# Optimization experiments

Measured on AMD Instinct MI355X. Metric: run time of the kernel, lower is better.

The kernel has to match this reference:

```python
import jax, jax.numpy as jnp
import numpy as np

COST_MASK = 5.0
COST_DICE = 5.0
COST_BOX = 5.0
COST_GIOU = 2.0


def point_sample(masks, pts):
    # masks: [N, H, W]; pts: [P, 2] with (x, y) in [0, 1].
    # Matches F.grid_sample(bilinear, align_corners=False, padding_mode='zeros')
    N, H, W = masks.shape
    x = pts[:, 0] * W - 0.5
    y = pts[:, 1] * H - 0.5
    x0 = jnp.floor(x)
    y0 = jnp.floor(y)
    wx = x - x0
    wy = y - y0
    x0i = x0.astype(jnp.int32)
    y0i = y0.astype(jnp.int32)

    def gather(yi, xi):
        valid = ((xi >= 0) & (xi < W) & (yi >= 0) & (yi < H)).astype(masks.dtype)
        v = masks[:, jnp.clip(yi, 0, H - 1), jnp.clip(xi, 0, W - 1)]  # [N, P]
        return v * valid

    v00 = gather(y0i, x0i)
    v01 = gather(y0i, x0i + 1)
    v10 = gather(y0i + 1, x0i)
    v11 = gather(y0i + 1, x0i + 1)
    return (v00 * (1 - wy) * (1 - wx) + v01 * (1 - wy) * wx
            + v10 * wy * (1 - wx) + v11 * wy * wx)  # [N, P]


def box_cxcywh_to_xyxy(b):
    cx, cy, w, h = b[..., 0], b[..., 1], b[..., 2], b[..., 3]
    return jnp.stack([cx - 0.5 * w, cy - 0.5 * h, cx + 0.5 * w, cy + 0.5 * h], axis=-1)


def generalized_box_iou(a, b):
    # a: [Q, 4], b: [T, 4] in xyxy
    area_a = (a[:, 2] - a[:, 0]) * (a[:, 3] - a[:, 1])
    area_b = (b[:, 2] - b[:, 0]) * (b[:, 3] - b[:, 1])
    lt = jnp.maximum(a[:, None, :2], b[None, :, :2])
    rb = jnp.minimum(a[:, None, 2:], b[None, :, 2:])
    wh = jnp.clip(rb - lt, 0.0)
    inter = wh[..., 0] * wh[..., 1]
    union = area_a[:, None] + area_b[None, :] - inter
    iou = inter / union
    lt_e = jnp.minimum(a[:, None, :2], b[None, :, :2])
    rb_e = jnp.maximum(a[:, None, 2:], b[None, :, 2:])
    wh_e = jnp.clip(rb_e - lt_e, 0.0)
    area_e = wh_e[..., 0] * wh_e[..., 1]
    return iou - (area_e - union) / area_e


def _cost_one(out_mask, tgt_mask, out_box, tgt_box, pts):
    om = point_sample(out_mask, pts)  # [Q, P] logits
    tm = point_sample(tgt_mask, pts)  # [T, P] binary targets
    P = om.shape[1]
    # batch_sigmoid_ce_loss: BCE(x,1)=softplus(-x), BCE(x,0)=softplus(x)
    pos = jax.nn.softplus(-om)
    neg = jax.nn.softplus(om)
    cost_mask = (jnp.einsum('qp,tp->qt', pos, tm)
                 + jnp.einsum('qp,tp->qt', neg, 1.0 - tm)) / P
    # batch_dice_loss
    s = jax.nn.sigmoid(om)
    numerator = 2.0 * jnp.einsum('qp,tp->qt', s, tm)
    denominator = s.sum(-1)[:, None] + tm.sum(-1)[None, :]
    cost_dice = 1.0 - (numerator + 1.0) / (denominator + 1.0)
    # box costs
    cost_bbox = jnp.abs(out_box[:, None, :] - tgt_box[None, :, :]).sum(-1)
    cost_giou = -generalized_box_iou(box_cxcywh_to_xyxy(out_box),
                                     box_cxcywh_to_xyxy(tgt_box))
    return (COST_MASK * cost_mask + COST_DICE * cost_dice
            + COST_BOX * cost_bbox + COST_GIOU * cost_giou)


def setup_inputs() -> dict:
    key = jax.random.key(0)
    k1, k2, k3, k4, k5 = jax.random.split(key, 5)
    B, Q, T, H, W, P = 2, 300, 300, 256, 256, 12544
    pred_masks = jax.random.normal(k1, (B, Q, H, W), dtype=jnp.float32)
    tgt_masks = (jax.random.uniform(k2, (B, T, H, W)) > 0.5).astype(jnp.float32)
    u = jax.random.uniform(k3, (B, Q, 4), dtype=jnp.float32)
    pred_boxes = jnp.concatenate([0.2 + 0.6 * u[..., :2], 0.05 + 0.25 * u[..., 2:]], axis=-1)
    v = jax.random.uniform(k4, (B, T, 4), dtype=jnp.float32)
    tgt_boxes = jnp.concatenate([0.2 + 0.6 * v[..., :2], 0.05 + 0.25 * v[..., 2:]], axis=-1)
    point_coords = jax.random.uniform(k5, (B, P, 2), dtype=jnp.float32)
    return {"pred_masks": pred_masks, "tgt_masks": tgt_masks,
            "pred_boxes": pred_boxes, "tgt_boxes": tgt_boxes,
            "point_coords": point_coords}


def reference(pred_masks, tgt_masks, pred_boxes, tgt_boxes, point_coords):
    # Batched cost matrix C: [B, Q, T]
    return jax.vmap(_cost_one)(pred_masks, tgt_masks, pred_boxes, tgt_boxes, point_coords)
```

## Files before the change

### kernel.cpp

```cpp
#include <hip/hip_runtime.h>
#include <hip/hip_bf16.h>
#include <math.h>

#define BB 2
#define QQ 300
#define TT 300
#define HH 256
#define WW 256
#define PP 12544
#define NCHUNK 16
#define PBLK (PP / 256)
#define NSPLIT 14

typedef __bf16 bf16_t;
typedef bf16_t bf16x8 __attribute__((ext_vector_type(8)));
typedef float floatx4 __attribute__((ext_vector_type(4)));

__device__ inline void gl_lds16(const void* g, void* l) {
    __builtin_amdgcn_global_load_lds(
        (const __attribute__((address_space(1))) unsigned int*)g,
        (__attribute__((address_space(3))) unsigned int*)l, 16, 0, 0);
}

#define LG_BAR() do {                                      \
    __builtin_amdgcn_sched_barrier(0);                     \
    asm volatile("s_waitcnt lgkmcnt(0)" ::: "memory");     \
    __builtin_amdgcn_s_barrier();                          \
    __builtin_amdgcn_sched_barrier(0);                     \
} while (0)

#define VM_BAR(N) do {                                     \
    __builtin_amdgcn_sched_barrier(0);                     \
    asm volatile("s_waitcnt vmcnt(" #N ")" ::: "memory");  \
    __builtin_amdgcn_s_barrier();                          \
    __builtin_amdgcn_sched_barrier(0);                     \
} while (0)

__global__ __launch_bounds__(256) void prep_kernel(const float* __restrict__ pts,
                                                   int4* __restrict__ off,
                                                   float4* __restrict__ wgt,
                                                   int* __restrict__ bkt,
                                                   int* __restrict__ hist) {
    __shared__ int lh[NCHUNK];
    int tid = threadIdx.x;
    if (tid < NCHUNK) lh[tid] = 0;
    __syncthreads();
    int idx = blockIdx.x * 256 + tid;
    int b = blockIdx.x / PBLK;
    float px = pts[idx * 2 + 0];
    float py = pts[idx * 2 + 1];
    float x = px * WW - 0.5f;
    float y = py * HH - 0.5f;
    float x0f = floorf(x), y0f = floorf(y);
    float wx = x - x0f, wy = y - y0f;
    int x0 = (int)x0f, y0 = (int)y0f;
    int x1 = x0 + 1, y1 = y0 + 1;
    float vx0 = (x0 >= 0 && x0 < WW) ? 1.f : 0.f;
    float vx1 = (x1 >= 0 && x1 < WW) ? 1.f : 0.f;
    float vy0 = (y0 >= 0 && y0 < HH) ? 1.f : 0.f;
    float vy1 = (y1 >= 0 && y1 < HH) ? 1.f : 0.f;
    int cx0 = min(max(x0, 0), WW - 1), cx1 = min(max(x1, 0), WW - 1);
    int cy0 = min(max(y0, 0), HH - 1), cy1 = min(max(y1, 0), HH - 1);
    off[idx] = make_int4(cy0 * WW + cx0, cy0 * WW + cx1, cy1 * WW + cx0, cy1 * WW + cx1);
    wgt[idx] = make_float4((1.f - wy) * (1.f - wx) * vy0 * vx0,
                           (1.f - wy) * wx        * vy0 * vx1,
                           wy        * (1.f - wx) * vy1 * vx0,
                           wy        * wx         * vy1 * vx1);
    int k = min(max(y0, 0), HH - 2) >> 4;
    bkt[idx] = k;
    atomicAdd(&lh[k], 1);
    __syncthreads();
    if (tid < NCHUNK && lh[tid] > 0) atomicAdd(&hist[b * NCHUNK + tid], lh[tid]);
}

__global__ void scan_kernel(const int* __restrict__ hist, int* __restrict__ cs,
                            int* __restrict__ ctr) {
    int b = threadIdx.x;
    if (b < BB) {
        int run = 0;
        for (int k = 0; k < NCHUNK; ++k) {
            cs[b * (NCHUNK + 1) + k] = run;
            ctr[b * NCHUNK + k] = run;
            run += hist[b * NCHUNK + k];
        }
        cs[b * (NCHUNK + 1) + NCHUNK] = run;
    }
}

__global__ __launch_bounds__(256) void scatter_kernel(const int4* __restrict__ off,
                                                      const float4* __restrict__ wgt,
                                                      const int* __restrict__ bkt,
                                                      int* __restrict__ ctr,
                                                      int4* __restrict__ off_s,
                                                      float4* __restrict__ wgt_s) {
    __shared__ int lh[NCHUNK];
    __shared__ int lbase[NCHUNK];
    int tid = threadIdx.x;
    if (tid < NCHUNK) lh[tid] = 0;
    __syncthreads();
    int idx = blockIdx.x * 256 + tid;
    int b = blockIdx.x / PBLK;
    int k = bkt[idx];
    int rank = atomicAdd(&lh[k], 1);
    __syncthreads();
    if (tid < NCHUNK) lbase[tid] = (lh[tid] > 0) ? atomicAdd(&ctr[b * NCHUNK + tid], lh[tid]) : 0;
    __syncthreads();
    int pos = lbase[k] + rank;
    off_s[b * PP + pos] = off[idx];
    wgt_s[b * PP + pos] = wgt[idx];
}

__global__ __launch_bounds__(256) void sample_kernel(
    const float* __restrict__ pred_masks, const float* __restrict__ tgt_masks,
    const int4* __restrict__ off_s, const float4* __restrict__ wgt_s,
    const int* __restrict__ cs_g,
    bf16_t* __restrict__ OM, bf16_t* __restrict__ TM,
    float* __restrict__ RS_SP, float* __restrict__ RS_S, float* __restrict__ RS_T) {
    int b = blockIdx.z;
    int m = blockIdx.x;
    int c = blockIdx.y;
    int tid = threadIdx.x;
    int wave = tid >> 6, lane = tid & 63;
    __shared__ __align__(16) float rows[17 * WW];
    __shared__ float ra_[4], rb_[4];

    bool is_pred = (m < QQ);
    const float* img;
    bf16_t* row0;
    if (is_pred) {
        img  = pred_masks + (size_t)(b * QQ + m) * (HH * WW);
        row0 = OM + (size_t)(b * QQ + m) * PP;
    } else {
        int t = m - QQ;
        img  = tgt_masks + (size_t)(b * TT + t) * (HH * WW);
        row0 = TM + (size_t)(b * TT + t) * PP;
    }

    int base = c * 16;
    const float4* gsrc = (const float4*)(img + base * WW);
    float4 p0 = gsrc[(wave + 0) * 64 + lane];
    float4 p1 = gsrc[(wave + 4) * 64 + lane];
    float4 p2 = gsrc[(wave + 8) * 64 + lane];
    float4 p3 = gsrc[(wave + 12) * 64 + lane];
    float4 p4;
    bool has17 = (c < NCHUNK - 1);
    if (has17 && wave == 0) p4 = gsrc[16 * 64 + lane];

    const int4*   offb = off_s + b * PP;
    const float4* wb   = wgt_s + b * PP;
    const int*    cs   = cs_g + b * (NCHUNK + 1);
    int j1 = cs[c + 1];
    int j = cs[c] + tid;
    int4 o; float4 w;
    if (j < j1) { o = offb[j]; w = wb[j]; }

    float4* d = (float4*)rows;
    d[(wave + 0) * 64 + lane] = p0;
    d[(wave + 4) * 64 + lane] = p1;
    d[(wave + 8) * 64 + lane] = p2;
    d[(wave + 12) * 64 + lane] = p3;
    if (has17 && wave == 0) d[16 * 64 + lane] = p4;
    __syncthreads();

    int boff = base * WW;
    float s0 = 0.f, s1 = 0.f;
    while (j < j1) {
        int jn = j + 256;
        int4 on; float4 wn;
        if (jn < j1) { on = offb[jn]; wn = wb[jn]; }
        float v = w.x * rows[o.x - boff] + w.y * rows[o.y - boff] +
                  w.z * rows[o.z - boff] + w.w * rows[o.w - boff];
        row0[j] = (bf16_t)v;
        if (is_pred) {
            float e = __expf(-fabsf(v));
            float r = 1.f / (1.f + e);
            float sg = (v >= 0.f) ? r : e * r;
            s0 += fmaxf(v, 0.f) + __logf(1.f + e);
            s1 += sg;
        } else {
            s0 += v;
        }
        o = on; w = wn; j = jn;
    }

    for (int sh = 32; sh > 0; sh >>= 1) {
        s0 += __shfl_down(s0, sh, 64);
        s1 += __shfl_down(s1, sh, 64);
    }
    if (lane == 0) { ra_[wave] = s0; rb_[wave] = s1; }
    __syncthreads();
    if (tid == 0) {
        float t0 = ra_[0] + ra_[1] + ra_[2] + ra_[3];
        float t1 = rb_[0] + rb_[1] + rb_[2] + rb_[3];
        if (is_pred) {
            atomicAdd(&RS_SP[b * QQ + m], t0);
            atomicAdd(&RS_S[b * QQ + m], t1);
        } else {
            atomicAdd(&RS_T[b * TT + (m - QQ)], t0);
        }
    }
}

__device__ inline bf16x8 sigmoid8(bf16x8 a) {
    bf16x8 r;
#pragma unroll
    for (int i = 0; i < 8; ++i) {
        float x = (float)a[i];
        float e = __expf(-fabsf(x));
        float q = 1.f / (1.f + e);
        r[i] = (bf16_t)((x >= 0.f) ? q : e * q);
    }
    return r;
}

template<int NS>
__global__ __launch_bounds__(512) void matmul_kernel(
    const bf16_t* __restrict__ OM, const bf16_t* __restrict__ TM,
    float* __restrict__ A1P, float* __restrict__ A2P) {
    constexpr int KSP = PP / NS;
    constexpr int KST = KSP / 64;
    static_assert(KSP % 64 == 0, "K split must be a multiple of 64");
    int b = blockIdx.z / NS;
    int split = blockIdx.z % NS;
    int m0 = blockIdx.x * 128;
    int n0 = blockIdx.y * 128;
    int tid = threadIdx.x;
    int wave = tid >> 6, lane = tid & 63;
    int lrow = lane & 15, quad = lane >> 4;
    int wm = wave & 3;
    int wn = wave >> 2;

    __shared__ __align__(16) bf16_t lds[2][2 * 128 * 64];

    int k0 = split * KSP;
    int lr8 = lane >> 3;
    int clog = (lane & 7) ^ lr8;

    const char* gp[4];
    unsigned lofs[4];
#pragma unroll
    for (int jj = 0; jj < 4; ++jj) {
        int L = wave + jj * 8;
        int mat = L >> 4, i = L & 15;
        int rb_ = mat ? n0 : m0;
        int row = min(rb_ + i * 8 + lr8, mat ? (TT - 1) : (QQ - 1));
        const bf16_t* g = mat ? TM + (size_t)b * TT * PP : OM + (size_t)b * QQ * PP;
        gp[jj] = (const char*)(g + (size_t)row * PP + k0) + clog * 16;
        lofs[jj] = mat * 8192 + i * 512;
    }

    floatx4 acc1[2][4], acc2[2][4];
#pragma unroll
    for (int r = 0; r < 2; ++r)
#pragma unroll
        for (int j = 0; j < 4; ++j) {
            acc1[r][j] = (floatx4){0.f, 0.f, 0.f, 0.f};
            acc2[r][j] = (floatx4){0.f, 0.f, 0.f, 0.f};
        }

#pragma unroll
    for (int jj = 0; jj < 4; ++jj) { gl_lds16(gp[jj], lds[0] + lofs[jj]); gp[jj] += 128; }

    int ar0 = wm * 32 + lrow;
    int ar1 = ar0 + 16;
    int ax0 = ar0 & 7, ax1 = ar1 & 7;
    for (int s = 0; s < KST; ++s) {
        if (s + 1 < KST) {
#pragma unroll
            for (int jj = 0; jj < 4; ++jj) { gl_lds16(gp[jj], lds[(s + 1) & 1] + lofs[jj]); gp[jj] += 128; }
            VM_BAR(4);
        } else {
            VM_BAR(0);
        }
        const bf16_t* Lp = lds[s & 1];
#pragma unroll
        for (int kk8 = 0; kk8 <= 4; kk8 += 4) {
            bf16x8 a1_0 = *(const bf16x8*)(Lp + ar0 * 64 + (((quad + kk8) ^ ax0) << 3));
            bf16x8 a1_1 = *(const bf16x8*)(Lp + ar1 * 64 + (((quad + kk8) ^ ax1) << 3));
            bf16x8 a2_0 = sigmoid8(a1_0);
            bf16x8 a2_1 = sigmoid8(a1_1);
#pragma unroll
            for (int j = 0; j < 4; ++j) {
                int br = wn * 64 + j * 16 + lrow;
                bf16x8 vb = *(const bf16x8*)(Lp + 8192 + br * 64 + (((quad + kk8) ^ (br & 7)) << 3));
                acc1[0][j] = __builtin_amdgcn_mfma_f32_16x16x32_bf16(a1_0, vb, acc1[0][j], 0, 0, 0);
                acc1[1][j] = __builtin_amdgcn_mfma_f32_16x16x32_bf16(a1_1, vb, acc1[1][j], 0, 0, 0);
                acc2[0][j] = __builtin_amdgcn_mfma_f32_16x16x32_bf16(a2_0, vb, acc2[0][j], 0, 0, 0);
                acc2[1][j] = __builtin_amdgcn_mfma_f32_16x16x32_bf16(a2_1, vb, acc2[1][j], 0, 0, 0);
            }
        }
        LG_BAR();
    }

    float* o1 = A1P + (size_t)(b * NS + split) * (QQ * TT);
    float* o2 = A2P + (size_t)(b * NS + split) * (QQ * TT);
#pragma unroll
    for (int r16 = 0; r16 < 2; ++r16) {
        int mrow = m0 + wm * 32 + r16 * 16 + quad * 4;
#pragma unroll
        for (int j = 0; j < 4; ++j) {
            int n = n0 + wn * 64 + j * 16 + lrow;
            if (n < TT) {
#pragma unroll
                for (int r = 0; r < 4; ++r) {
                    int mm = mrow + r;
                    if (mm < QQ) {
                        o1[mm * TT + n] = acc1[r16][j][r];
                        o2[mm * TT + n] = acc2[r16][j][r];
                    }
                }
            }
        }
    }
}

template<int NS>
__global__ __launch_bounds__(256) void combine_kernel(
    const float* __restrict__ A1P, const float* __restrict__ A2P,
    const float* __restrict__ RS_SP, const float* __restrict__ RS_S, const float* __restrict__ RS_T,
    const float* __restrict__ pred_boxes, const float* __restrict__ tgt_boxes,
    float* __restrict__ out) {
    int idx = blockIdx.x * 256 + threadIdx.x;
    if (idx >= BB * QQ * TT) return;
    int b = idx / (QQ * TT);
    int r = idx - b * (QQ * TT);
    int q = r / TT;
    int t = r - q * TT;

    float a1 = 0.f, a2 = 0.f;
    for (int s = 0; s < NS; ++s) {
        a1 += A1P[(size_t)(b * NS + s) * (QQ * TT) + r];
        a2 += A2P[(size_t)(b * NS + s) * (QQ * TT) + r];
    }
    float cm = (RS_SP[b * QQ + q] - a1) * (1.0f / (float)PP);
    float cd = 1.f - (2.f * a2 + 1.f) / (RS_S[b * QQ + q] + RS_T[b * TT + t] + 1.f);

    const float* pb = pred_boxes + (size_t)(b * QQ + q) * 4;
    const float* tb = tgt_boxes + (size_t)(b * TT + t) * 4;
    float cb = fabsf(pb[0] - tb[0]) + fabsf(pb[1] - tb[1]) +
               fabsf(pb[2] - tb[2]) + fabsf(pb[3] - tb[3]);

    float ax0 = pb[0] - 0.5f * pb[2], ay0 = pb[1] - 0.5f * pb[3];
    float ax1 = pb[0] + 0.5f * pb[2], ay1 = pb[1] + 0.5f * pb[3];
    float bx0 = tb[0] - 0.5f * tb[2], by0 = tb[1] - 0.5f * tb[3];
    float bx1 = tb[0] + 0.5f * tb[2], by1 = tb[1] + 0.5f * tb[3];
    float area_a = (ax1 - ax0) * (ay1 - ay0);
    float area_b = (bx1 - bx0) * (by1 - by0);
    float iw = fmaxf(fminf(ax1, bx1) - fmaxf(ax0, bx0), 0.f);
    float ih = fmaxf(fminf(ay1, by1) - fmaxf(ay0, by0), 0.f);
    float inter = iw * ih;
    float uni = area_a + area_b - inter;
    float iou = inter / uni;
    float ew = fmaxf(ax1, bx1) - fminf(ax0, bx0);
    float eh = fmaxf(ay1, by1) - fminf(ay0, by0);
    float area_e = ew * eh;
    float giou = iou - (area_e - uni) / area_e;

    out[idx] = 5.f * cm + 5.f * cd + 5.f * cb - 2.f * giou;
}

extern "C" void kernel_launch(void* const* d_in, const int* in_sizes, int n_in,
                              void* d_out, int out_size, void* d_ws, size_t ws_size,
                              hipStream_t stream) {
    const float* pred_masks = (const float*)d_in[0];
    const float* tgt_masks  = (const float*)d_in[1];
    const float* pred_boxes = (const float*)d_in[2];
    const float* tgt_boxes  = (const float*)d_in[3];
    const float* pts        = (const float*)d_in[4];

    char* w = (char*)d_ws;
    auto alloc = [&](size_t bytes) -> char* {
        char* r = w;
        w += (bytes + 255) & ~(size_t)255;
        return r;
    };
    int4*   OFF   = (int4*)  alloc((size_t)BB * PP * sizeof(int4));
    float4* WGT   = (float4*)alloc((size_t)BB * PP * sizeof(float4));
    int*    BKT   = (int*)   alloc((size_t)BB * PP * sizeof(int));
    int4*   OFF_S = (int4*)  alloc((size_t)BB * PP * sizeof(int4));
    float4* WGT_S = (float4*)alloc((size_t)BB * PP * sizeof(float4));
    int*    CS    = (int*)   alloc((size_t)BB * (NCHUNK + 1) * sizeof(int));
    bf16_t* OM    = (bf16_t*)alloc((size_t)BB * QQ * PP * 2);
    bf16_t* TM    = (bf16_t*)alloc((size_t)BB * TT * PP * 2);
    float*  RS_SP = (float*) alloc((size_t)BB * QQ * 4);
    float*  RS_S  = (float*) alloc((size_t)BB * QQ * 4);
    float*  RS_T  = (float*) alloc((size_t)BB * TT * 4);
    int*    HIST  = (int*)   alloc((size_t)BB * NCHUNK * sizeof(int));
    int*    CTR   = (int*)   alloc((size_t)BB * NCHUNK * sizeof(int));
    float*  A1P   = (float*) alloc((size_t)BB * NSPLIT * QQ * TT * 4);
    float*  A2P   = (float*) alloc((size_t)BB * NSPLIT * QQ * TT * 4);

    hipMemsetAsync(RS_SP, 0, (size_t)((char*)A1P - (char*)RS_SP), stream);

    prep_kernel<<<BB * PBLK, 256, 0, stream>>>(pts, OFF, WGT, BKT, HIST);
    scan_kernel<<<1, 64, 0, stream>>>(HIST, CS, CTR);
    scatter_kernel<<<BB * PBLK, 256, 0, stream>>>(OFF, WGT, BKT, CTR, OFF_S, WGT_S);
    sample_kernel<<<dim3(QQ + TT, NCHUNK, BB), 256, 0, stream>>>(
        pred_masks, tgt_masks, OFF_S, WGT_S, CS, OM, TM, RS_SP, RS_S, RS_T);
    matmul_kernel<NSPLIT><<<dim3(3, 3, BB * NSPLIT), 512, 0, stream>>>(OM, TM, A1P, A2P);
    combine_kernel<NSPLIT><<<(BB * QQ * TT + 255) / 256, 256, 0, stream>>>(
        A1P, A2P, RS_SP, RS_S, RS_T, pred_boxes, tgt_boxes, (float*)d_out);
}
```

Measured before the change: 393.2 us.

## Reduce split-K partials with atomics and double the K split count

The matmul now accumulates split-K partial results into a single zeroed buffer per batch using float atomicAdd, instead of writing NSPLIT separate partial matrices that the combine kernel summed. The split count is raised from 14 to 28 so the grid has more workgroups, and the combine kernel reads only one value per element. This removes the large partial-buffer writes and reads and the serial reduction loop. In exchange it adds atomic contention across 28 splits and makes the summation order nondeterministic.

```diff
diff --git a/kernel.cpp b/kernel.cpp
--- a/kernel.cpp
+++ b/kernel.cpp
@@ -10,7 +10,7 @@
 #define PP 12544
 #define NCHUNK 16
 #define PBLK (PP / 256)
-#define NSPLIT 14
+#define NSPLIT 28
 
 typedef __bf16 bf16_t;
 typedef bf16_t bf16x8 __attribute__((ext_vector_type(8)));
@@ -216,7 +216,7 @@
 template<int NS>
 __global__ __launch_bounds__(512) void matmul_kernel(
     const bf16_t* __restrict__ OM, const bf16_t* __restrict__ TM,
-    float* __restrict__ A1P, float* __restrict__ A2P) {
+    float* __restrict__ A1, float* __restrict__ A2) {
     constexpr int KSP = PP / NS;
     constexpr int KST = KSP / 64;
     static_assert(KSP % 64 == 0, "K split must be a multiple of 64");
@@ -292,8 +292,8 @@
         LG_BAR();
     }
 
-    float* o1 = A1P + (size_t)(b * NS + split) * (QQ * TT);
-    float* o2 = A2P + (size_t)(b * NS + split) * (QQ * TT);
+    float* o1 = A1 + (size_t)b * (QQ * TT);
+    float* o2 = A2 + (size_t)b * (QQ * TT);
 #pragma unroll
     for (int r16 = 0; r16 < 2; ++r16) {
         int mrow = m0 + wm * 32 + r16 * 16 + quad * 4;
@@ -305,8 +305,8 @@
                 for (int r = 0; r < 4; ++r) {
                     int mm = mrow + r;
                     if (mm < QQ) {
-                        o1[mm * TT + n] = acc1[r16][j][r];
-                        o2[mm * TT + n] = acc2[r16][j][r];
+                        atomicAdd(&o1[mm * TT + n], acc1[r16][j][r]);
+                        atomicAdd(&o2[mm * TT + n], acc2[r16][j][r]);
                     }
                 }
             }
@@ -314,9 +314,8 @@
     }
 }
 
-template<int NS>
 __global__ __launch_bounds__(256) void combine_kernel(
-    const float* __restrict__ A1P, const float* __restrict__ A2P,
+    const float* __restrict__ A1, const float* __restrict__ A2,
     const float* __restrict__ RS_SP, const float* __restrict__ RS_S, const float* __restrict__ RS_T,
     const float* __restrict__ pred_boxes, const float* __restrict__ tgt_boxes,
     float* __restrict__ out) {
@@ -327,11 +326,8 @@
     int q = r / TT;
     int t = r - q * TT;
 
-    float a1 = 0.f, a2 = 0.f;
-    for (int s = 0; s < NS; ++s) {
-        a1 += A1P[(size_t)(b * NS + s) * (QQ * TT) + r];
-        a2 += A2P[(size_t)(b * NS + s) * (QQ * TT) + r];
-    }
+    float a1 = A1[idx];
+    float a2 = A2[idx];
     float cm = (RS_SP[b * QQ + q] - a1) * (1.0f / (float)PP);
     float cd = 1.f - (2.f * a2 + 1.f) / (RS_S[b * QQ + q] + RS_T[b * TT + t] + 1.f);
 
@@ -387,17 +383,17 @@
     float*  RS_T  = (float*) alloc((size_t)BB * TT * 4);
     int*    HIST  = (int*)   alloc((size_t)BB * NCHUNK * sizeof(int));
     int*    CTR   = (int*)   alloc((size_t)BB * NCHUNK * sizeof(int));
-    float*  A1P   = (float*) alloc((size_t)BB * NSPLIT * QQ * TT * 4);
-    float*  A2P   = (float*) alloc((size_t)BB * NSPLIT * QQ * TT * 4);
-
-    hipMemsetAsync(RS_SP, 0, (size_t)((char*)A1P - (char*)RS_SP), stream);
+    float*  A1    = (float*) alloc((size_t)BB * QQ * TT * 4);
+    float*  A2    = (float*) alloc((size_t)BB * QQ * TT * 4);
+
+    hipMemsetAsync(RS_SP, 0, (size_t)(w - (char*)RS_SP), stream);
 
     prep_kernel<<<BB * PBLK, 256, 0, stream>>>(pts, OFF, WGT, BKT, HIST);
     scan_kernel<<<1, 64, 0, stream>>>(HIST, CS, CTR);
     scatter_kernel<<<BB * PBLK, 256, 0, stream>>>(OFF, WGT, BKT, CTR, OFF_S, WGT_S);
     sample_kernel<<<dim3(QQ + TT, NCHUNK, BB), 256, 0, stream>>>(
         pred_masks, tgt_masks, OFF_S, WGT_S, CS, OM, TM, RS_SP, RS_S, RS_T);
-    matmul_kernel<NSPLIT><<<dim3(3, 3, BB * NSPLIT), 512, 0, stream>>>(OM, TM, A1P, A2P);
-    combine_kernel<NSPLIT><<<(BB * QQ * TT + 255) / 256, 256, 0, stream>>>(
-        A1P, A2P, RS_SP, RS_S, RS_T, pred_boxes, tgt_boxes, (float*)d_out);
-}
+    matmul_kernel<NSPLIT><<<dim3(3, 3, BB * NSPLIT), 512, 0, stream>>>(OM, TM, A1, A2);
+    combine_kernel<<<(BB * QQ * TT + 255) / 256, 256, 0, stream>>>(
+        A1, A2, RS_SP, RS_S, RS_T, pred_boxes, tgt_boxes, (float*)d_out);
+}
```

New measurement: 433.2 us. 10.2% more time.
